# Kernel tuning notes

Hardware: AMD Instinct MI355X
Metric: run time of the kernel (lower is better)

Reference implementation:

```python
import jax, jax.numpy as jnp
import numpy as np

B, CQ, CKV, H, W = 8, 256, 512, 64, 64
HKV, WKV = 32, 32
DQK = CQ // 8  # 32


def setup_inputs() -> dict:
    key = jax.random.key(0)
    ks = jax.random.split(key, 9)
    s = 0.05
    return {
        "query": jax.random.normal(ks[0], (B, CQ, H, W), jnp.float32),
        "key_value": jax.random.normal(ks[1], (B, CKV, HKV, WKV), jnp.float32),
        "Wq": jax.random.normal(ks[2], (DQK, CQ), jnp.float32) * s,
        "bq": jax.random.normal(ks[3], (DQK,), jnp.float32) * s,
        "Wk": jax.random.normal(ks[4], (DQK, CKV), jnp.float32) * s,
        "bk": jax.random.normal(ks[5], (DQK,), jnp.float32) * s,
        "Wv": jax.random.normal(ks[6], (CQ, CKV), jnp.float32) * s,
        "bv": jax.random.normal(ks[7], (CQ,), jnp.float32) * s,
        "gamma": jax.random.normal(ks[8], (1,), jnp.float32) * 0.5,
    }


def reference(query, key_value, Wq, bq, Wk, bk, Wv, bv, gamma):
    b, cq, h, w = query.shape
    n = h * w
    # bilinear resize of key_value to query's spatial size (align_corners=False
    # half-pixel convention, matching torch F.interpolate and jax.image.resize)
    kv = jax.image.resize(key_value, (b, key_value.shape[1], h, w), method="bilinear")
    # 1x1 convs are channel contractions
    q = jnp.einsum("bchw,dc->bdhw", query, Wq) + bq[None, :, None, None]   # [B,DQK,H,W]
    k = jnp.einsum("bchw,dc->bdhw", kv, Wk) + bk[None, :, None, None]      # [B,DQK,H,W]
    v = jnp.einsum("bchw,dc->bdhw", kv, Wv) + bv[None, :, None, None]      # [B,CQ,H,W]
    qf = q.reshape(b, -1, n)   # [B,DQK,N]
    kf = k.reshape(b, -1, n)   # [B,DQK,N]
    vf = v.reshape(b, -1, n)   # [B,CQ,N]
    energy = jnp.einsum("bdn,bdm->bnm", qf, kf)        # [B,N,N]
    attention = jax.nn.softmax(energy, axis=-1)
    out = jnp.einsum("bnm,bcm->bcn", attention, vf)     # [B,CQ,N]
    out = out.reshape(b, cq, h, w)
    return gamma[0] * out + query
```

## Files before the change

kernel.cpp:

```cpp
#include <hip/hip_runtime.h>

#define B_ 8
#define CQ_ 256
#define CKV_ 512
#define N_ 4096
#define DQK_ 32

typedef __bf16 bf16;
typedef __bf16 bf16x8 __attribute__((ext_vector_type(8)));
typedef float f32x4 __attribute__((ext_vector_type(4)));

__global__ void k_convert_w(const float* __restrict__ Wq, const float* __restrict__ Wk,
                            const float* __restrict__ Wv,
                            bf16* __restrict__ wq, bf16* __restrict__ wk, bf16* __restrict__ wv) {
    int i = blockIdx.x * 256 + threadIdx.x;
    if (i < 8192) wq[i] = (bf16)Wq[i];
    else if (i < 24576) wk[i - 8192] = (bf16)Wk[i - 8192];
    else if (i < 155648) wv[i - 24576] = (bf16)Wv[i - 24576];
}

__global__ __launch_bounds__(256) void k_resize(const float* __restrict__ kv, bf16* __restrict__ kvr) {
    const int yo = blockIdx.x;
    const int b  = blockIdx.y;
    const int tid = threadIdx.x;
    __shared__ float r0[64][33];
    __shared__ float r1[64][33];
    int ty = yo >> 1;
    int y0, y1; float wy0, wy1;
    if ((yo & 1) == 0) { y0 = ty > 0 ? ty - 1 : 0; y1 = ty; wy0 = 0.25f; wy1 = 0.75f; }
    else               { y0 = ty; y1 = ty < 31 ? ty + 1 : 31; wy0 = 0.75f; wy1 = 0.25f; }
    const int u_loc = tid & 63;
    const int xo_base = tid >> 6;
    for (int uc = 0; uc < CKV_; uc += 64) {
        __syncthreads();
        for (int i = 0; i < 8; ++i) {
            int idx = tid + i * 256;
            int u = idx >> 5, x = idx & 31;
            const float* src = kv + ((size_t)b * CKV_ + uc + u) * 1024 + x;
            r0[u][x] = src[y0 * 32];
            r1[u][x] = src[y1 * 32];
        }
        __syncthreads();
        for (int i = 0; i < 16; ++i) {
            int xo = xo_base + i * 4;
            int tx = xo >> 1;
            int xa, xb; float wxa, wxb;
            if ((xo & 1) == 0) { xa = tx > 0 ? tx - 1 : 0; xb = tx; wxa = 0.25f; wxb = 0.75f; }
            else               { xa = tx; xb = tx < 31 ? tx + 1 : 31; wxa = 0.75f; wxb = 0.25f; }
            float v0 = wxa * r0[u_loc][xa] + wxb * r0[u_loc][xb];
            float v1 = wxa * r1[u_loc][xa] + wxb * r1[u_loc][xb];
            float val = wy0 * v0 + wy1 * v1;
            kvr[((size_t)b * N_ + yo * 64 + xo) * CKV_ + uc + u_loc] = (bf16)val;
        }
    }
}

__global__ __launch_bounds__(256) void k_transpose_q(const float* __restrict__ q, bf16* __restrict__ qryT) {
    const int nb = blockIdx.x * 64;
    const int cb = blockIdx.y * 64;
    const int b  = blockIdx.z;
    const int tid = threadIdx.x;
    __shared__ float tile[64][65];
    const int col = tid & 63, row4 = tid >> 6;
    for (int i = 0; i < 16; ++i) {
        int r = row4 + i * 4;
        tile[r][col] = q[((size_t)b * CQ_ + cb + r) * N_ + nb + col];
    }
    __syncthreads();
    for (int i = 0; i < 16; ++i) {
        int r = row4 + i * 4;
        qryT[((size_t)b * N_ + nb + r) * CQ_ + cb + col] = (bf16)tile[col][r];
    }
}

template <int K>
__global__ __launch_bounds__(256) void k_proj_qk(const bf16* __restrict__ W,
                                                 const float* __restrict__ bias,
                                                 const bf16* __restrict__ Bm,
                                                 bf16* __restrict__ outT) {
    const int mb = blockIdx.x * 128;
    const int b  = blockIdx.y;
    const int tid = threadIdx.x;
    const int w = tid >> 6, lane = tid & 63;
    const int l16 = lane & 15, quad = lane >> 4;
    const int ct = w & 1;
    const int mhalf = (w >> 1) * 64;
    f32x4 acc[4];
    for (int j = 0; j < 4; ++j) acc[j] = (f32x4){0.f, 0.f, 0.f, 0.f};
    const bf16* aptr  = W + (ct * 16 + l16) * K + quad * 8;
    const bf16* bbase = Bm + ((size_t)b * N_ + mb + mhalf) * K + quad * 8;
#pragma unroll
    for (int ks = 0; ks < K / 32; ++ks) {
        bf16x8 af = *(const bf16x8*)(aptr + ks * 32);
        for (int j = 0; j < 4; ++j) {
            bf16x8 bfv = *(const bf16x8*)(bbase + (size_t)(j * 16 + l16) * K + ks * 32);
            acc[j] = __builtin_amdgcn_mfma_f32_16x16x32_bf16(af, bfv, acc[j], 0, 0, 0);
        }
    }
    for (int j = 0; j < 4; ++j)
        for (int r = 0; r < 4; ++r) {
            int d = ct * 16 + quad * 4 + r;
            int m = mb + mhalf + j * 16 + l16;
            outT[((size_t)b * N_ + m) * DQK_ + d] = (bf16)(acc[j][r] + bias[d]);
        }
}

__global__ __launch_bounds__(256) void k_proj_v(const bf16* __restrict__ W,
                                                const float* __restrict__ bias,
                                                const bf16* __restrict__ Bm,
                                                bf16* __restrict__ vout) {
    const int mb = blockIdx.x * 64;
    const int b  = blockIdx.y;
    const int tid = threadIdx.x;
    const int w = tid >> 6, lane = tid & 63;
    const int l16 = lane & 15, quad = lane >> 4;
    f32x4 acc[4][4];
    for (int i = 0; i < 4; ++i) for (int j = 0; j < 4; ++j) acc[i][j] = (f32x4){0.f, 0.f, 0.f, 0.f};
    const bf16* bbase = Bm + ((size_t)b * N_ + mb) * CKV_ + quad * 8;
#pragma unroll 4
    for (int ks = 0; ks < 16; ++ks) {
        bf16x8 bfv[4];
        for (int j = 0; j < 4; ++j)
            bfv[j] = *(const bf16x8*)(bbase + (size_t)(j * 16 + l16) * CKV_ + ks * 32);
        for (int i = 0; i < 4; ++i) {
            bf16x8 af = *(const bf16x8*)(W + (size_t)((w * 4 + i) * 16 + l16) * CKV_ + ks * 32 + quad * 8);
            for (int j = 0; j < 4; ++j)
                acc[i][j] = __builtin_amdgcn_mfma_f32_16x16x32_bf16(af, bfv[j], acc[i][j], 0, 0, 0);
        }
    }
    for (int i = 0; i < 4; ++i)
        for (int r = 0; r < 4; ++r) {
            int c = (w * 4 + i) * 16 + quad * 4 + r;
            float bvs = bias[c];
            for (int j = 0; j < 4; ++j) {
                int m = mb + j * 16 + l16;
                vout[((size_t)b * CQ_ + c) * N_ + m] = (bf16)(acc[i][j][r] + bvs);
            }
        }
}

__global__ __launch_bounds__(256) void k_flash(const bf16* __restrict__ qT,
                                               const bf16* __restrict__ kT,
                                               const bf16* __restrict__ vv,
                                               const float* __restrict__ query,
                                               const float* __restrict__ gamma,
                                               float* __restrict__ out) {
    __shared__ bf16 P[2][64][72];
    __shared__ float lrow[64];
    const int b  = blockIdx.y;
    const int n0 = blockIdx.x * 64;
    const int tid = threadIdx.x;
    const int w = tid >> 6, lane = tid & 63;
    const int l16 = lane & 15, quad = lane >> 4;

    bf16x8 qfrag = *(const bf16x8*)(qT + ((size_t)b * N_ + n0 + w * 16 + l16) * DQK_ + quad * 8);

    f32x4 acc[4][4];
    for (int i = 0; i < 4; ++i) for (int j = 0; j < 4; ++j) acc[i][j] = (f32x4){0.f, 0.f, 0.f, 0.f};
    float lsum[4] = {0.f, 0.f, 0.f, 0.f};

    const bf16* kbase = kT + (size_t)b * N_ * DQK_;
    const bf16* vbase = vv + ((size_t)b * CQ_ + w * 64) * N_;

    for (int mt = 0; mt < 64; ++mt) {
        const int m0 = mt * 64;
        bf16x8 vf[2][4];
        for (int ks = 0; ks < 2; ++ks)
            for (int i = 0; i < 4; ++i)
                vf[ks][i] = *(const bf16x8*)(vbase + (size_t)(i * 16 + l16) * N_ + m0 + ks * 32 + quad * 8);
        float pv[4][4];
        for (int i = 0; i < 4; ++i) {
            bf16x8 kf = *(const bf16x8*)(kbase + (size_t)(m0 + i * 16 + l16) * DQK_ + quad * 8);
            f32x4 s = __builtin_amdgcn_mfma_f32_16x16x32_bf16(qfrag, kf, (f32x4){0.f, 0.f, 0.f, 0.f}, 0, 0, 0);
            for (int r = 0; r < 4; ++r) {
                float p = __expf(s[r]);
                pv[i][r] = p;
                lsum[r] += p;
            }
        }
        bf16 (* __restrict__ Pb)[72] = P[mt & 1];
        for (int i = 0; i < 4; ++i)
            for (int r = 0; r < 4; ++r)
                Pb[w * 16 + quad * 4 + r][i * 16 + l16] = (bf16)pv[i][r];
        __syncthreads();
        for (int ks = 0; ks < 2; ++ks) {
            bf16x8 pf[4];
            for (int j = 0; j < 4; ++j)
                pf[j] = *(const bf16x8*)&Pb[j * 16 + l16][ks * 32 + quad * 8];
            for (int i = 0; i < 4; ++i)
                for (int j = 0; j < 4; ++j)
                    acc[i][j] = __builtin_amdgcn_mfma_f32_16x16x32_bf16(vf[ks][i], pf[j], acc[i][j], 0, 0, 0);
        }
    }
    for (int off = 1; off < 16; off <<= 1)
        for (int r = 0; r < 4; ++r)
            lsum[r] += __shfl_xor(lsum[r], off, 16);
    if (l16 == 0)
        for (int r = 0; r < 4; ++r) lrow[w * 16 + quad * 4 + r] = lsum[r];
    __syncthreads();
    const float g = gamma[0];
    float linv[4];
    for (int j = 0; j < 4; ++j) linv[j] = 1.f / lrow[j * 16 + l16];
    for (int i = 0; i < 4; ++i)
        for (int r = 0; r < 4; ++r) {
            int c = w * 64 + i * 16 + quad * 4 + r;
            for (int j = 0; j < 4; ++j) {
                int n = n0 + j * 16 + l16;
                size_t idx = ((size_t)b * CQ_ + c) * N_ + n;
                out[idx] = g * acc[i][j][r] * linv[j] + query[idx];
            }
        }
}

extern "C" void kernel_launch(void* const* d_in, const int* in_sizes, int n_in,
                              void* d_out, int out_size, void* d_ws, size_t ws_size,
                              hipStream_t stream) {
    const float* query     = (const float*)d_in[0];
    const float* key_value = (const float*)d_in[1];
    const float* Wq = (const float*)d_in[2];
    const float* bq = (const float*)d_in[3];
    const float* Wk = (const float*)d_in[4];
    const float* bk = (const float*)d_in[5];
    const float* Wv = (const float*)d_in[6];
    const float* bv = (const float*)d_in[7];
    const float* gamma = (const float*)d_in[8];
    float* out = (float*)d_out;

    char* ws = (char*)d_ws;
    bf16* kvr  = (bf16*)(ws);
    bf16* qryT = (bf16*)(ws + 33554432);
    bf16* vbuf = (bf16*)(ws + 33554432);
    bf16* qTb  = (bf16*)(ws + 50331648);
    bf16* kTb  = (bf16*)(ws + 52428800);
    bf16* wqb  = (bf16*)(ws + 54525952);
    bf16* wkb  = (bf16*)(ws + 54542336);
    bf16* wvb  = (bf16*)(ws + 54575104);

    k_convert_w<<<608, 256, 0, stream>>>(Wq, Wk, Wv, wqb, wkb, wvb);
    k_resize<<<dim3(64, 8), 256, 0, stream>>>(key_value, kvr);
    k_transpose_q<<<dim3(64, 4, 8), 256, 0, stream>>>(query, qryT);
    k_proj_qk<256><<<dim3(32, 8), 256, 0, stream>>>(wqb, bq, qryT, qTb);
    k_proj_qk<512><<<dim3(32, 8), 256, 0, stream>>>(wkb, bk, kvr, kTb);
    k_proj_v<<<dim3(64, 8), 256, 0, stream>>>(wvb, bv, kvr, vbuf);
    k_flash<<<dim3(64, 8), 256, 0, stream>>>(qTb, kTb, vbuf, query, gamma, out);
}
```

Measured before the change: 352.0 us.

## Fuse query transpose into Q projection and split flash block across 8 waves

The separate transpose kernel and Q projection become one kernel that stages query in LDS as bf16 and runs the MFMA projection directly from the tile, removing one launch and the round trip of an intermediate buffer through global memory. The flash kernel grows to 512 threads. Each wave now computes half the score tiles and accumulates half the output columns, with row sums reduced across the two halves through shared memory. This halves per-wave accumulator registers and increases waves per block for latency hiding, at the cost of each wave loading V fragments redundantly.

```diff
diff --git a/kernel.cpp b/kernel.cpp
--- a/kernel.cpp
+++ b/kernel.cpp
@@ -7,6 +7,7 @@
 #define DQK_ 32
 
 typedef __bf16 bf16;
+typedef __bf16 bf16x4 __attribute__((ext_vector_type(4)));
 typedef __bf16 bf16x8 __attribute__((ext_vector_type(8)));
 typedef float f32x4 __attribute__((ext_vector_type(4)));
 
@@ -55,29 +56,50 @@
     }
 }
 
-__global__ __launch_bounds__(256) void k_transpose_q(const float* __restrict__ q, bf16* __restrict__ qryT) {
-    const int nb = blockIdx.x * 64;
-    const int cb = blockIdx.y * 64;
-    const int b  = blockIdx.z;
-    const int tid = threadIdx.x;
-    __shared__ float tile[64][65];
-    const int col = tid & 63, row4 = tid >> 6;
-    for (int i = 0; i < 16; ++i) {
-        int r = row4 + i * 4;
-        tile[r][col] = q[((size_t)b * CQ_ + cb + r) * N_ + nb + col];
+__global__ __launch_bounds__(256) void k_proj_q_fused(const float* __restrict__ query,
+                                                      const bf16* __restrict__ W,
+                                                      const float* __restrict__ bias,
+                                                      bf16* __restrict__ qTb) {
+    __shared__ bf16 tile[64][264];
+    const int n0 = blockIdx.x * 64;
+    const int b  = blockIdx.y;
+    const int tid = threadIdx.x;
+    const int xi = tid & 15, c0 = tid >> 4;
+    for (int pass = 0; pass < 16; ++pass) {
+        int c = c0 + pass * 16;
+        const float4 v = *(const float4*)(query + ((size_t)b * CQ_ + c) * N_ + n0 + xi * 4);
+        tile[xi * 4 + 0][c] = (bf16)v.x;
+        tile[xi * 4 + 1][c] = (bf16)v.y;
+        tile[xi * 4 + 2][c] = (bf16)v.z;
+        tile[xi * 4 + 3][c] = (bf16)v.w;
     }
     __syncthreads();
-    for (int i = 0; i < 16; ++i) {
-        int r = row4 + i * 4;
-        qryT[((size_t)b * N_ + nb + r) * CQ_ + cb + col] = (bf16)tile[col][r];
-    }
-}
-
-template <int K>
-__global__ __launch_bounds__(256) void k_proj_qk(const bf16* __restrict__ W,
-                                                 const float* __restrict__ bias,
-                                                 const bf16* __restrict__ Bm,
-                                                 bf16* __restrict__ outT) {
+    const int w = tid >> 6, lane = tid & 63;
+    const int l16 = lane & 15, quad = lane >> 4;
+    const int ct = w & 1, nh = w >> 1;
+    f32x4 acc[2];
+    acc[0] = (f32x4){0.f, 0.f, 0.f, 0.f}; acc[1] = (f32x4){0.f, 0.f, 0.f, 0.f};
+    const bf16* aptr = W + (ct * 16 + l16) * CQ_ + quad * 8;
+#pragma unroll
+    for (int ks = 0; ks < 8; ++ks) {
+        bf16x8 af = *(const bf16x8*)(aptr + ks * 32);
+        for (int j = 0; j < 2; ++j) {
+            bf16x8 bfv = *(const bf16x8*)&tile[nh * 32 + j * 16 + l16][ks * 32 + quad * 8];
+            acc[j] = __builtin_amdgcn_mfma_f32_16x16x32_bf16(af, bfv, acc[j], 0, 0, 0);
+        }
+    }
+    for (int j = 0; j < 2; ++j)
+        for (int r = 0; r < 4; ++r) {
+            int d = ct * 16 + quad * 4 + r;
+            int n = n0 + nh * 32 + j * 16 + l16;
+            qTb[((size_t)b * N_ + n) * DQK_ + d] = (bf16)(acc[j][r] + bias[d]);
+        }
+}
+
+__global__ __launch_bounds__(256) void k_proj_k(const bf16* __restrict__ W,
+                                                const float* __restrict__ bias,
+                                                const bf16* __restrict__ Bm,
+                                                bf16* __restrict__ outT) {
     const int mb = blockIdx.x * 128;
     const int b  = blockIdx.y;
     const int tid = threadIdx.x;
@@ -87,13 +109,13 @@
     const int mhalf = (w >> 1) * 64;
     f32x4 acc[4];
     for (int j = 0; j < 4; ++j) acc[j] = (f32x4){0.f, 0.f, 0.f, 0.f};
-    const bf16* aptr  = W + (ct * 16 + l16) * K + quad * 8;
-    const bf16* bbase = Bm + ((size_t)b * N_ + mb + mhalf) * K + quad * 8;
+    const bf16* aptr  = W + (ct * 16 + l16) * CKV_ + quad * 8;
+    const bf16* bbase = Bm + ((size_t)b * N_ + mb + mhalf) * CKV_ + quad * 8;
 #pragma unroll
-    for (int ks = 0; ks < K / 32; ++ks) {
+    for (int ks = 0; ks < 16; ++ks) {
         bf16x8 af = *(const bf16x8*)(aptr + ks * 32);
         for (int j = 0; j < 4; ++j) {
-            bf16x8 bfv = *(const bf16x8*)(bbase + (size_t)(j * 16 + l16) * K + ks * 32);
+            bf16x8 bfv = *(const bf16x8*)(bbase + (size_t)(j * 16 + l16) * CKV_ + ks * 32);
             acc[j] = __builtin_amdgcn_mfma_f32_16x16x32_bf16(af, bfv, acc[j], 0, 0, 0);
         }
     }
@@ -139,28 +161,32 @@
         }
 }
 
-__global__ __launch_bounds__(256) void k_flash(const bf16* __restrict__ qT,
-                                               const bf16* __restrict__ kT,
-                                               const bf16* __restrict__ vv,
-                                               const float* __restrict__ query,
-                                               const float* __restrict__ gamma,
-                                               float* __restrict__ out) {
+__global__ __launch_bounds__(512, 4) void k_flash(const bf16* __restrict__ qT,
+                                                  const bf16* __restrict__ kT,
+                                                  const bf16* __restrict__ vv,
+                                                  const float* __restrict__ query,
+                                                  const float* __restrict__ gamma,
+                                                  float* __restrict__ out) {
     __shared__ bf16 P[2][64][72];
-    __shared__ float lrow[64];
+    __shared__ float lred[2][4][16];
     const int b  = blockIdx.y;
     const int n0 = blockIdx.x * 64;
     const int tid = threadIdx.x;
-    const int w = tid >> 6, lane = tid & 63;
-    const int l16 = lane & 15, quad = lane >> 4;
-
-    bf16x8 qfrag = *(const bf16x8*)(qT + ((size_t)b * N_ + n0 + w * 16 + l16) * DQK_ + quad * 8);
-
-    f32x4 acc[4][4];
-    for (int i = 0; i < 4; ++i) for (int j = 0; j < 4; ++j) acc[i][j] = (f32x4){0.f, 0.f, 0.f, 0.f};
-    float lsum[4] = {0.f, 0.f, 0.f, 0.f};
+    const int w = tid >> 6;
+    const int lane = tid & 63, l16 = lane & 15, quad = lane >> 4;
+    const int jn   = w & 3;
+    const int half = w >> 2;
+    const int cb   = (w & 3) * 64;
+    const int nh   = half;
+
+    bf16x8 qfrag = *(const bf16x8*)(qT + ((size_t)b * N_ + n0 + jn * 16 + l16) * DQK_ + quad * 8);
+
+    f32x4 acc[4][2];
+    for (int i = 0; i < 4; ++i) for (int j = 0; j < 2; ++j) acc[i][j] = (f32x4){0.f, 0.f, 0.f, 0.f};
+    float lsum = 0.f;
 
     const bf16* kbase = kT + (size_t)b * N_ * DQK_;
-    const bf16* vbase = vv + ((size_t)b * CQ_ + w * 64) * N_;
+    const bf16* vbase = vv + ((size_t)b * CQ_ + cb) * N_;
 
     for (int mt = 0; mt < 64; ++mt) {
         const int m0 = mt * 64;
@@ -168,44 +194,42 @@
         for (int ks = 0; ks < 2; ++ks)
             for (int i = 0; i < 4; ++i)
                 vf[ks][i] = *(const bf16x8*)(vbase + (size_t)(i * 16 + l16) * N_ + m0 + ks * 32 + quad * 8);
-        float pv[4][4];
-        for (int i = 0; i < 4; ++i) {
-            bf16x8 kf = *(const bf16x8*)(kbase + (size_t)(m0 + i * 16 + l16) * DQK_ + quad * 8);
-            f32x4 s = __builtin_amdgcn_mfma_f32_16x16x32_bf16(qfrag, kf, (f32x4){0.f, 0.f, 0.f, 0.f}, 0, 0, 0);
+        bf16 (* __restrict__ Pb)[72] = P[mt & 1];
+        for (int ii = 0; ii < 2; ++ii) {
+            const int im = half * 2 + ii;
+            bf16x8 kf = *(const bf16x8*)(kbase + (size_t)(m0 + im * 16 + l16) * DQK_ + quad * 8);
+            f32x4 s = __builtin_amdgcn_mfma_f32_16x16x32_bf16(kf, qfrag, (f32x4){0.f, 0.f, 0.f, 0.f}, 0, 0, 0);
+            bf16x4 pk;
             for (int r = 0; r < 4; ++r) {
                 float p = __expf(s[r]);
-                pv[i][r] = p;
-                lsum[r] += p;
+                lsum += p;
+                pk[r] = (bf16)p;
             }
-        }
-        bf16 (* __restrict__ Pb)[72] = P[mt & 1];
-        for (int i = 0; i < 4; ++i)
-            for (int r = 0; r < 4; ++r)
-                Pb[w * 16 + quad * 4 + r][i * 16 + l16] = (bf16)pv[i][r];
+            *(bf16x4*)&Pb[jn * 16 + l16][im * 16 + quad * 4] = pk;
+        }
         __syncthreads();
         for (int ks = 0; ks < 2; ++ks) {
-            bf16x8 pf[4];
-            for (int j = 0; j < 4; ++j)
-                pf[j] = *(const bf16x8*)&Pb[j * 16 + l16][ks * 32 + quad * 8];
+            bf16x8 pf[2];
+            for (int j = 0; j < 2; ++j)
+                pf[j] = *(const bf16x8*)&Pb[(nh * 2 + j) * 16 + l16][ks * 32 + quad * 8];
             for (int i = 0; i < 4; ++i)
-                for (int j = 0; j < 4; ++j)
+                for (int j = 0; j < 2; ++j)
                     acc[i][j] = __builtin_amdgcn_mfma_f32_16x16x32_bf16(vf[ks][i], pf[j], acc[i][j], 0, 0, 0);
         }
     }
-    for (int off = 1; off < 16; off <<= 1)
-        for (int r = 0; r < 4; ++r)
-            lsum[r] += __shfl_xor(lsum[r], off, 16);
-    if (l16 == 0)
-        for (int r = 0; r < 4; ++r) lrow[w * 16 + quad * 4 + r] = lsum[r];
+    lsum += __shfl_xor(lsum, 16);
+    lsum += __shfl_xor(lsum, 32);
+    if (lane < 16) lred[half][jn][l16] = lsum;
     __syncthreads();
     const float g = gamma[0];
-    float linv[4];
-    for (int j = 0; j < 4; ++j) linv[j] = 1.f / lrow[j * 16 + l16];
+    float linv[2];
+    for (int j = 0; j < 2; ++j)
+        linv[j] = 1.f / (lred[0][nh * 2 + j][l16] + lred[1][nh * 2 + j][l16]);
     for (int i = 0; i < 4; ++i)
         for (int r = 0; r < 4; ++r) {
-            int c = w * 64 + i * 16 + quad * 4 + r;
-            for (int j = 0; j < 4; ++j) {
-                int n = n0 + j * 16 + l16;
+            int c = cb + i * 16 + quad * 4 + r;
+            for (int j = 0; j < 2; ++j) {
+                int n = n0 + (nh * 2 + j) * 16 + l16;
                 size_t idx = ((size_t)b * CQ_ + c) * N_ + n;
                 out[idx] = g * acc[i][j][r] * linv[j] + query[idx];
             }
@@ -228,7 +252,6 @@
 
     char* ws = (char*)d_ws;
     bf16* kvr  = (bf16*)(ws);
-    bf16* qryT = (bf16*)(ws + 33554432);
     bf16* vbuf = (bf16*)(ws + 33554432);
     bf16* qTb  = (bf16*)(ws + 50331648);
     bf16* kTb  = (bf16*)(ws + 52428800);
@@ -238,9 +261,8 @@
 
     k_convert_w<<<608, 256, 0, stream>>>(Wq, Wk, Wv, wqb, wkb, wvb);
     k_resize<<<dim3(64, 8), 256, 0, stream>>>(key_value, kvr);
-    k_transpose_q<<<dim3(64, 4, 8), 256, 0, stream>>>(query, qryT);
-    k_proj_qk<256><<<dim3(32, 8), 256, 0, stream>>>(wqb, bq, qryT, qTb);
-    k_proj_qk<512><<<dim3(32, 8), 256, 0, stream>>>(wkb, bk, kvr, kTb);
+    k_proj_q_fused<<<dim3(64, 8), 256, 0, stream>>>(query, wqb, bq, qTb);
+    k_proj_k<<<dim3(32, 8), 256, 0, stream>>>(wkb, bk, kvr, kTb);
     k_proj_v<<<dim3(64, 8), 256, 0, stream>>>(wvb, bv, kvr, vbuf);
-    k_flash<<<dim3(64, 8), 256, 0, stream>>>(qTb, kTb, vbuf, query, gamma, out);
-}
+    k_flash<<<dim3(64, 8), 512, 0, stream>>>(qTb, kTb, vbuf, query, gamma, out);
+}
```

After: 451.5 us. +28.2%, slower.
